# Optimization experiments

Hardware: AMD Instinct MI355X
Metric: run time of the kernel (lower is better)

## Reference

```python
import jax, jax.numpy as jnp
import numpy as np

B, N, D, H = 4, 2048, 768, 12
DH = D // H  # 64


def setup_inputs() -> dict:
    key = jax.random.key(0)
    k1, k2, k3 = jax.random.split(key, 3)
    x = jax.random.normal(k1, (B, N, D), dtype=jnp.float32)
    # causal mask, broadcastable over (b, h): 1 = keep, 0 = masked
    mask = jnp.tril(jnp.ones((N, N), dtype=jnp.int32))[None, None, :, :]
    w_qkv = jax.random.normal(k2, (D, 3 * D), dtype=jnp.float32) * 0.02
    w_out = jax.random.normal(k3, (D, D), dtype=jnp.float32) * 0.02
    return {"x": x, "mask": mask, "w_qkv": w_qkv, "w_out": w_out}


def reference(x, mask, w_qkv, w_out):
    b, n, d = x.shape
    qkv = x @ w_qkv                               # [b, n, 3d]
    q, k, v = jnp.split(qkv, 3, axis=-1)
    def to_heads(t):
        return t.reshape(b, n, H, DH).transpose(0, 2, 1, 3)  # [b, h, n, dh]
    q, k, v = to_heads(q), to_heads(k), to_heads(v)
    attn = jnp.einsum('bhqd,bhkd->bhqk', q, k) / jnp.sqrt(jnp.float32(DH))
    attn = jnp.where(mask == 0, -jnp.inf, attn)
    attn = jax.nn.softmax(attn.astype(jnp.float32), axis=-1).astype(x.dtype)
    out = jnp.einsum('bhqk,bhkd->bhqd', attn, v)  # [b, h, n, dh]
    out = out.transpose(0, 2, 1, 3).reshape(b, n, d)
    return out @ w_out
```

## Files before the change

kernel.cpp:

```cpp
#include <hip/hip_runtime.h>
#include <stdint.h>

#define B_  4
#define N_  2048
#define D_  768
#define H_  12
#define DH_ 64
#define TD  (3*D_)
#define M_  (B_*N_)

typedef __bf16 bf16x8 __attribute__((ext_vector_type(8)));
typedef float  f32x4  __attribute__((ext_vector_type(4)));
typedef unsigned int   u32x4 __attribute__((ext_vector_type(4)));
typedef unsigned short u16x4 __attribute__((ext_vector_type(4)));

__device__ __forceinline__ unsigned short f2bf(float f) {
  union { float f; uint32_t u; } c; c.f = f;
  uint32_t u = c.u;
  uint32_t r = (u + 0x7FFFu + ((u >> 16) & 1u)) >> 16;
  return (unsigned short)r;
}

template <bool A_BF16, bool OUT_BF16>
__global__ __launch_bounds__(256)
void gemm_kernel(const void* __restrict__ Av, const float* __restrict__ Bm,
                 void* __restrict__ Cv, int M, int N, int K,
                 float qscale, int qcols) {
  __shared__ unsigned short As[128 * 32];
  __shared__ unsigned short Bs[128 * 32];
  const int tid  = threadIdx.x;
  const int lane = tid & 63;
  const int wave = tid >> 6;
  const int wr = wave >> 1, wc = wave & 1;
  const int l15 = lane & 15, lh = lane >> 4;
  const int row0 = blockIdx.y * 128;
  const int col0 = blockIdx.x * 128;

  f32x4 acc[4][4] = {};

  for (int k0 = 0; k0 < K; k0 += 32) {
    if constexpr (A_BF16) {
      const unsigned short* A = (const unsigned short*)Av;
      #pragma unroll
      for (int it = 0; it < 2; ++it) {
        int idx = tid + it * 256;
        int r = idx >> 2, c8 = idx & 3;
        u32x4 v = *(const u32x4*)(A + (size_t)(row0 + r) * K + k0 + c8 * 8);
        *(u32x4*)(As + r * 32 + ((c8 * 8) ^ ((r & 6) << 2))) = v;
      }
    } else {
      const float* A = (const float*)Av;
      #pragma unroll
      for (int it = 0; it < 4; ++it) {
        int idx = tid + it * 256;
        int r = idx >> 3, c4 = idx & 7;
        f32x4 v = *(const f32x4*)(A + (size_t)(row0 + r) * K + k0 + c4 * 4);
        u16x4 hx; hx.x = f2bf(v.x); hx.y = f2bf(v.y); hx.z = f2bf(v.z); hx.w = f2bf(v.w);
        *(u16x4*)(As + r * 32 + ((c4 * 4) ^ ((r & 6) << 2))) = hx;
      }
    }
    #pragma unroll
    for (int it = 0; it < 4; ++it) {
      int idx = tid + it * 256;
      int n = idx & 127, kq = idx >> 7;
      float f0 = Bm[(size_t)(k0 + kq * 4 + 0) * N + col0 + n];
      float f1 = Bm[(size_t)(k0 + kq * 4 + 1) * N + col0 + n];
      float f2 = Bm[(size_t)(k0 + kq * 4 + 2) * N + col0 + n];
      float f3 = Bm[(size_t)(k0 + kq * 4 + 3) * N + col0 + n];
      u16x4 hx; hx.x = f2bf(f0); hx.y = f2bf(f1); hx.z = f2bf(f2); hx.w = f2bf(f3);
      *(u16x4*)(Bs + n * 32 + ((kq * 4) ^ ((n & 6) << 2))) = hx;
    }
    __syncthreads();

    bf16x8 af[4], bfv[4];
    #pragma unroll
    for (int mf = 0; mf < 4; ++mf) {
      int rr = wr * 64 + mf * 16 + l15;
      af[mf] = *(const bf16x8*)(As + rr * 32 + ((lh * 8) ^ ((rr & 6) << 2)));
    }
    #pragma unroll
    for (int nf = 0; nf < 4; ++nf) {
      int n = wc * 64 + nf * 16 + l15;
      bfv[nf] = *(const bf16x8*)(Bs + n * 32 + ((lh * 8) ^ ((n & 6) << 2)));
    }
    __builtin_amdgcn_s_setprio(1);
    #pragma unroll
    for (int mf = 0; mf < 4; ++mf)
      #pragma unroll
      for (int nf = 0; nf < 4; ++nf)
        acc[mf][nf] = __builtin_amdgcn_mfma_f32_16x16x32_bf16(af[mf], bfv[nf], acc[mf][nf], 0, 0, 0);
    __builtin_amdgcn_s_setprio(0);
    __syncthreads();
  }

  #pragma unroll
  for (int mf = 0; mf < 4; ++mf) {
    #pragma unroll
    for (int nf = 0; nf < 4; ++nf) {
      #pragma unroll
      for (int rg = 0; rg < 4; ++rg) {
        int rr = row0 + wr * 64 + mf * 16 + lh * 4 + rg;
        int cc = col0 + wc * 64 + nf * 16 + l15;
        float v = acc[mf][nf][rg];
        if (cc < qcols) v *= qscale;
        if constexpr (OUT_BF16) ((unsigned short*)Cv)[(size_t)rr * N + cc] = f2bf(v);
        else                    ((float*)Cv)[(size_t)rr * N + cc] = v;
      }
    }
  }
}

__global__ __launch_bounds__(256)
void attn_kernel(const unsigned short* __restrict__ qkv,
                 float* __restrict__ Oacc, float* __restrict__ Lacc) {
  __shared__ unsigned short Ks[2][64 * 64];
  __shared__ unsigned short Vs[2][64 * 64];
  __shared__ unsigned short Ps[4 * 32 * 64];
  const int tid  = threadIdx.x;
  const int lane = tid & 63, wave = tid >> 6;
  const int l15 = lane & 15, lh = lane >> 4;

  const int g = blockIdx.x;
  const int j = g >> 3;
  const int bh = (j / 40) * 8 + (g & 7);
  const int r = j % 40;
  const int b = bh / H_, h = bh % H_;
  const short cum[17] = {0,1,2,3,4,6,8,10,12,15,18,21,24,28,32,36,40};
  int qb = 15;
  #pragma unroll
  for (int q = 15; q > 0; --q) if (r < cum[q]) qb = q - 1;
  const int chunk = r - cum[qb];
  const int t0 = chunk * 8;
  const int t1 = min(t0 + 8, 2 * (qb + 1));
  const int q0 = qb * 128 + wave * 32;

  bf16x8 qf[2][2];
  #pragma unroll
  for (int mf = 0; mf < 2; ++mf)
    #pragma unroll
    for (int ks = 0; ks < 2; ++ks)
      qf[mf][ks] = *(const bf16x8*)(qkv + (size_t)(b * N_ + q0 + mf * 16 + l15) * TD
                                    + h * DH_ + ks * 32 + lh * 8);

  f32x4 o[2][4] = {};
  float ls[2][4] = {};

  u32x4 kr[2], vr[2];
  const int s_kv = tid >> 3, s_d8 = tid & 7;

  auto ISSUE = [&](int t) {
    #pragma unroll
    for (int it = 0; it < 2; ++it) {
      int kv = s_kv + it * 32;
      size_t base = (size_t)(b * N_ + t * 64 + kv) * TD + h * DH_ + s_d8 * 8;
      kr[it] = *(const u32x4*)(qkv + base + D_);
      vr[it] = *(const u32x4*)(qkv + base + 2 * D_);
    }
  };
  auto WRITE = [&](int buf) {
    #pragma unroll
    for (int it = 0; it < 2; ++it) {
      int kv = s_kv + it * 32;
      *(u32x4*)(&Ks[buf][kv * 64 + ((s_d8 * 8) ^ ((kv & 7) << 3))]) = kr[it];
      const unsigned short* vsp = (const unsigned short*)&vr[it];
      #pragma unroll
      for (int jj = 0; jj < 8; ++jj) {
        int d = s_d8 * 8 + jj;
        int swz = (jj ^ s_d8) & 7;
        Vs[buf][d * 64 + (kv ^ (swz << 3))] = vsp[jj];
      }
    }
  };

  ISSUE(t0); WRITE(0); __syncthreads();

  for (int t = t0; t < t1; ++t) {
    const int cur = (t - t0) & 1;
    const bool more = (t + 1 < t1);
    if (more) ISSUE(t + 1);

    const int kv0 = t * 64;
    if (kv0 <= q0 + 31) {
      f32x4 s[2][4] = {};
      __builtin_amdgcn_s_setprio(1);
      #pragma unroll
      for (int ks = 0; ks < 2; ++ks) {
        bf16x8 kf[4];
        #pragma unroll
        for (int nf = 0; nf < 4; ++nf) {
          int kv = nf * 16 + l15;
          kf[nf] = *(const bf16x8*)(&Ks[cur][kv * 64 + ((ks * 32 + lh * 8) ^ ((kv & 7) << 3))]);
        }
        #pragma unroll
        for (int mf = 0; mf < 2; ++mf)
          #pragma unroll
          for (int nf = 0; nf < 4; ++nf)
            s[mf][nf] = __builtin_amdgcn_mfma_f32_16x16x32_bf16(qf[mf][ks], kf[nf], s[mf][nf], 0, 0, 0);
      }
      __builtin_amdgcn_s_setprio(0);

      const bool need_mask = (kv0 + 63 > q0);
      #pragma unroll
      for (int mf = 0; mf < 2; ++mf) {
        #pragma unroll
        for (int rg = 0; rg < 4; ++rg) {
          const int row = q0 + mf * 16 + lh * 4 + rg;
          const int prow = mf * 16 + lh * 4 + rg;
          float lacc = 0.f;
          #pragma unroll
          for (int nf = 0; nf < 4; ++nf) {
            int col = kv0 + nf * 16 + l15;
            float p = exp2f(s[mf][nf][rg]);
            if (need_mask && col > row) p = 0.f;
            lacc += p;
            Ps[wave * 2048 + prow * 64 + ((nf * 16 + l15) ^ ((prow & 7) << 3))] = f2bf(p);
          }
          ls[mf][rg] += lacc;
        }
      }

      __builtin_amdgcn_s_setprio(1);
      #pragma unroll
      for (int ks = 0; ks < 2; ++ks) {
        bf16x8 pf[2], vf[4];
        #pragma unroll
        for (int mf = 0; mf < 2; ++mf) {
          int pr = mf * 16 + l15;
          pf[mf] = *(const bf16x8*)(&Ps[wave * 2048 + pr * 64 + ((ks * 32 + lh * 8) ^ ((pr & 7) << 3))]);
        }
        #pragma unroll
        for (int nf = 0; nf < 4; ++nf) {
          int d = nf * 16 + l15;
          int swz = ((d & 7) ^ ((d >> 3) & 7)) & 7;
          vf[nf] = *(const bf16x8*)(&Vs[cur][d * 64 + ((ks * 32 + lh * 8) ^ (swz << 3))]);
        }
        #pragma unroll
        for (int mf = 0; mf < 2; ++mf)
          #pragma unroll
          for (int nf = 0; nf < 4; ++nf)
            o[mf][nf] = __builtin_amdgcn_mfma_f32_16x16x32_bf16(pf[mf], vf[nf], o[mf][nf], 0, 0, 0);
      }
      __builtin_amdgcn_s_setprio(0);
    }

    if (more) WRITE(cur ^ 1);
    __syncthreads();
  }

  #pragma unroll
  for (int mf = 0; mf < 2; ++mf)
    #pragma unroll
    for (int rg = 0; rg < 4; ++rg) {
      float v = ls[mf][rg];
      v += __shfl_xor(v, 1); v += __shfl_xor(v, 2);
      v += __shfl_xor(v, 4); v += __shfl_xor(v, 8);
      ls[mf][rg] = v;
    }
  if (l15 == 0) {
    #pragma unroll
    for (int rg = 0; rg < 4; ++rg)
      atomicAdd(&Lacc[(size_t)(b * N_ + q0 + lh * 4 + rg) * H_ + h], ls[0][rg]);
  } else if (l15 == 8) {
    #pragma unroll
    for (int rg = 0; rg < 4; ++rg)
      atomicAdd(&Lacc[(size_t)(b * N_ + q0 + 16 + lh * 4 + rg) * H_ + h], ls[1][rg]);
  }
  #pragma unroll
  for (int mf = 0; mf < 2; ++mf)
    #pragma unroll
    for (int rg = 0; rg < 4; ++rg) {
      int row = q0 + mf * 16 + lh * 4 + rg;
      #pragma unroll
      for (int nf = 0; nf < 4; ++nf)
        atomicAdd(&Oacc[(size_t)(b * N_ + row) * D_ + h * DH_ + nf * 16 + l15], o[mf][nf][rg]);
    }
}

__global__ __launch_bounds__(256)
void norm_kernel(const float* __restrict__ Oacc, const float* __restrict__ Lacc,
                 unsigned short* __restrict__ ctx) {
  int e8 = blockIdx.x * 256 + threadIdx.x;
  int row = e8 / 96, c8 = e8 % 96;
  int h = c8 >> 3;
  float inv = 1.f / Lacc[(size_t)row * H_ + h];
  const float* src = Oacc + (size_t)row * D_ + c8 * 8;
  f32x4 a = *(const f32x4*)(src);
  f32x4 bb = *(const f32x4*)(src + 4);
  u16x4 lo, hi;
  lo.x = f2bf(a.x * inv); lo.y = f2bf(a.y * inv); lo.z = f2bf(a.z * inv); lo.w = f2bf(a.w * inv);
  hi.x = f2bf(bb.x * inv); hi.y = f2bf(bb.y * inv); hi.z = f2bf(bb.z * inv); hi.w = f2bf(bb.w * inv);
  unsigned short* dst = ctx + (size_t)row * D_ + c8 * 8;
  *(u16x4*)(dst) = lo;
  *(u16x4*)(dst + 4) = hi;
}

extern "C" void kernel_launch(void* const* d_in, const int* in_sizes, int n_in,
                              void* d_out, int out_size, void* d_ws, size_t ws_size,
                              hipStream_t stream) {
  const float* x     = (const float*)d_in[0];
  const float* w_qkv = (const float*)d_in[2];
  const float* w_out = (const float*)d_in[3];

  char* ws = (char*)d_ws;
  unsigned short* qkv = (unsigned short*)ws;
  unsigned short* ctx = (unsigned short*)(ws + 37748736);
  float* Lacc         = (float*)(ws + 50331648);
  float* Oacc = (float*)d_out;
  float* out  = (float*)d_out;

  const float SC = 0.18033688011112042f;
  hipMemsetAsync(Oacc, 0, 25165824, stream);
  hipMemsetAsync(Lacc, 0, 393216, stream);

  dim3 blk(256);
  gemm_kernel<false, true><<<dim3(TD / 128, M_ / 128), blk, 0, stream>>>(
      x, w_qkv, qkv, M_, TD, D_, SC, D_);
  attn_kernel<<<dim3(48 * 40), blk, 0, stream>>>(qkv, Oacc, Lacc);
  norm_kernel<<<dim3(M_ * 96 / 256), blk, 0, stream>>>(Oacc, Lacc, ctx);
  gemm_kernel<true, false><<<dim3(D_ / 128, M_ / 128), blk, 0, stream>>>(
      ctx, w_out, out, M_, D_, D_, 1.0f, 0);
}
```

Baseline: 310.8 us.

## Pre-convert inputs to bf16, transpose weights, use direct global-to-LDS GEMM loads

Adds pre-pass kernels that convert x to bf16 and transpose and convert both weight matrices to bf16, folding the Q scale into the transposed QKV weights. The two GEMMs become a single bf16 kernel with both operands K-contiguous, loaded by global_load_lds straight into LDS with a 64-wide K step and an XOR swizzle. This removes the strided fp32 weight gathers and per-element conversions from the GEMM inner loop. It costs three extra launches and more workspace, and it stages x_bf in the output buffer, which is zeroed only after the first GEMM has read it.

```diff
diff --git a/kernel.cpp b/kernel.cpp
--- a/kernel.cpp
+++ b/kernel.cpp
@@ -21,13 +21,55 @@
   return (unsigned short)r;
 }
 
-template <bool A_BF16, bool OUT_BF16>
-__global__ __launch_bounds__(256)
-void gemm_kernel(const void* __restrict__ Av, const float* __restrict__ Bm,
-                 void* __restrict__ Cv, int M, int N, int K,
-                 float qscale, int qcols) {
-  __shared__ unsigned short As[128 * 32];
-  __shared__ unsigned short Bs[128 * 32];
+__device__ __forceinline__ void gload16(const unsigned short* g, unsigned short* l) {
+  __builtin_amdgcn_global_load_lds(
+      (const __attribute__((address_space(1))) void*)g,
+      (__attribute__((address_space(3))) void*)l, 16, 0, 0);
+}
+
+__global__ __launch_bounds__(256)
+void convx_kernel(const float* __restrict__ x, unsigned short* __restrict__ xb) {
+  int i = (blockIdx.x * 256 + threadIdx.x) * 8;
+  f32x4 a = *(const f32x4*)(x + i);
+  f32x4 b = *(const f32x4*)(x + i + 4);
+  u16x4 lo, hi;
+  lo.x = f2bf(a.x); lo.y = f2bf(a.y); lo.z = f2bf(a.z); lo.w = f2bf(a.w);
+  hi.x = f2bf(b.x); hi.y = f2bf(b.y); hi.z = f2bf(b.z); hi.w = f2bf(b.w);
+  *(u16x4*)(xb + i) = lo;
+  *(u16x4*)(xb + i + 4) = hi;
+}
+
+__global__ __launch_bounds__(256)
+void convwT_kernel(const float* __restrict__ W, unsigned short* __restrict__ WT,
+                   int R, int C, float sc, int qcols) {
+  __shared__ float tile[32][33];
+  const int C0 = blockIdx.x * 32, R0 = blockIdx.y * 32;
+  const int t = threadIdx.x;
+  {
+    int r = t >> 3, c4 = (t & 7) * 4;
+    f32x4 v = *(const f32x4*)(W + (size_t)(R0 + r) * C + C0 + c4);
+    tile[r][c4] = v.x; tile[r][c4 + 1] = v.y; tile[r][c4 + 2] = v.z; tile[r][c4 + 3] = v.w;
+  }
+  __syncthreads();
+  {
+    int n = t >> 3, r4 = (t & 7) * 4;
+    float s = (C0 + n) < qcols ? sc : 1.0f;
+    u16x4 o;
+    o.x = f2bf(tile[r4][n] * s);
+    o.y = f2bf(tile[r4 + 1][n] * s);
+    o.z = f2bf(tile[r4 + 2][n] * s);
+    o.w = f2bf(tile[r4 + 3][n] * s);
+    *(u16x4*)(WT + (size_t)(C0 + n) * R + R0 + r4) = o;
+  }
+}
+
+template <bool OUT_BF16>
+__global__ __launch_bounds__(256)
+void gemm_bt_kernel(const unsigned short* __restrict__ A,
+                    const unsigned short* __restrict__ BT,
+                    void* __restrict__ Cv, int M, int N, int K) {
+  __shared__ unsigned short As[128 * 64];
+  __shared__ unsigned short Bs[128 * 64];
   const int tid  = threadIdx.x;
   const int lane = tid & 63;
   const int wave = tid >> 6;
@@ -36,60 +78,52 @@
   const int row0 = blockIdx.y * 128;
   const int col0 = blockIdx.x * 128;
 
+  const unsigned short* ga[4];
+  const unsigned short* gb[4];
+  unsigned short* la = As + wave * 2048;
+  unsigned short* lb = Bs + wave * 2048;
+  #pragma unroll
+  for (int q = 0; q < 4; ++q) {
+    int rl = 32 * wave + 8 * q + (lane >> 3);
+    int kb = (((lane & 7) << 4) ^ ((rl & 7) << 4)) >> 1;
+    ga[q] = A  + (size_t)(row0 + rl) * K + kb;
+    gb[q] = BT + (size_t)(col0 + rl) * K + kb;
+  }
+
   f32x4 acc[4][4] = {};
 
-  for (int k0 = 0; k0 < K; k0 += 32) {
-    if constexpr (A_BF16) {
-      const unsigned short* A = (const unsigned short*)Av;
-      #pragma unroll
-      for (int it = 0; it < 2; ++it) {
-        int idx = tid + it * 256;
-        int r = idx >> 2, c8 = idx & 3;
-        u32x4 v = *(const u32x4*)(A + (size_t)(row0 + r) * K + k0 + c8 * 8);
-        *(u32x4*)(As + r * 32 + ((c8 * 8) ^ ((r & 6) << 2))) = v;
-      }
-    } else {
-      const float* A = (const float*)Av;
-      #pragma unroll
-      for (int it = 0; it < 4; ++it) {
-        int idx = tid + it * 256;
-        int r = idx >> 3, c4 = idx & 7;
-        f32x4 v = *(const f32x4*)(A + (size_t)(row0 + r) * K + k0 + c4 * 4);
-        u16x4 hx; hx.x = f2bf(v.x); hx.y = f2bf(v.y); hx.z = f2bf(v.z); hx.w = f2bf(v.w);
-        *(u16x4*)(As + r * 32 + ((c4 * 4) ^ ((r & 6) << 2))) = hx;
-      }
-    }
-    #pragma unroll
-    for (int it = 0; it < 4; ++it) {
-      int idx = tid + it * 256;
-      int n = idx & 127, kq = idx >> 7;
-      float f0 = Bm[(size_t)(k0 + kq * 4 + 0) * N + col0 + n];
-      float f1 = Bm[(size_t)(k0 + kq * 4 + 1) * N + col0 + n];
-      float f2 = Bm[(size_t)(k0 + kq * 4 + 2) * N + col0 + n];
-      float f3 = Bm[(size_t)(k0 + kq * 4 + 3) * N + col0 + n];
-      u16x4 hx; hx.x = f2bf(f0); hx.y = f2bf(f1); hx.z = f2bf(f2); hx.w = f2bf(f3);
-      *(u16x4*)(Bs + n * 32 + ((kq * 4) ^ ((n & 6) << 2))) = hx;
+  for (int k0 = 0; k0 < K; k0 += 64) {
+    #pragma unroll
+    for (int q = 0; q < 4; ++q) {
+      gload16(ga[q], la + q * 512);
+      gload16(gb[q], lb + q * 512);
+      ga[q] += 64; gb[q] += 64;
     }
     __syncthreads();
 
-    bf16x8 af[4], bfv[4];
-    #pragma unroll
-    for (int mf = 0; mf < 4; ++mf) {
-      int rr = wr * 64 + mf * 16 + l15;
-      af[mf] = *(const bf16x8*)(As + rr * 32 + ((lh * 8) ^ ((rr & 6) << 2)));
-    }
-    #pragma unroll
-    for (int nf = 0; nf < 4; ++nf) {
-      int n = wc * 64 + nf * 16 + l15;
-      bfv[nf] = *(const bf16x8*)(Bs + n * 32 + ((lh * 8) ^ ((n & 6) << 2)));
-    }
-    __builtin_amdgcn_s_setprio(1);
-    #pragma unroll
-    for (int mf = 0; mf < 4; ++mf)
-      #pragma unroll
-      for (int nf = 0; nf < 4; ++nf)
-        acc[mf][nf] = __builtin_amdgcn_mfma_f32_16x16x32_bf16(af[mf], bfv[nf], acc[mf][nf], 0, 0, 0);
-    __builtin_amdgcn_s_setprio(0);
+    #pragma unroll
+    for (int ks = 0; ks < 2; ++ks) {
+      bf16x8 af[4], bfv[4];
+      #pragma unroll
+      for (int mf = 0; mf < 4; ++mf) {
+        int r = wr * 64 + mf * 16 + l15;
+        af[mf] = *(const bf16x8*)((const char*)As +
+                  ((r * 128 + ks * 64 + lh * 16) ^ ((r & 7) << 4)));
+      }
+      #pragma unroll
+      for (int nf = 0; nf < 4; ++nf) {
+        int n = wc * 64 + nf * 16 + l15;
+        bfv[nf] = *(const bf16x8*)((const char*)Bs +
+                  ((n * 128 + ks * 64 + lh * 16) ^ ((n & 7) << 4)));
+      }
+      __builtin_amdgcn_s_setprio(1);
+      #pragma unroll
+      for (int mf = 0; mf < 4; ++mf)
+        #pragma unroll
+        for (int nf = 0; nf < 4; ++nf)
+          acc[mf][nf] = __builtin_amdgcn_mfma_f32_16x16x32_bf16(af[mf], bfv[nf], acc[mf][nf], 0, 0, 0);
+      __builtin_amdgcn_s_setprio(0);
+    }
     __syncthreads();
   }
 
@@ -102,7 +136,6 @@
         int rr = row0 + wr * 64 + mf * 16 + lh * 4 + rg;
         int cc = col0 + wc * 64 + nf * 16 + l15;
         float v = acc[mf][nf][rg];
-        if (cc < qcols) v *= qscale;
         if constexpr (OUT_BF16) ((unsigned short*)Cv)[(size_t)rr * N + cc] = f2bf(v);
         else                    ((float*)Cv)[(size_t)rr * N + cc] = v;
       }
@@ -305,18 +338,22 @@
   unsigned short* qkv = (unsigned short*)ws;
   unsigned short* ctx = (unsigned short*)(ws + 37748736);
   float* Lacc         = (float*)(ws + 50331648);
+  unsigned short* wTq = (unsigned short*)(ws + 50724864);
+  unsigned short* wTo = (unsigned short*)(ws + 54263808);
+  unsigned short* x_bf = (unsigned short*)d_out;
   float* Oacc = (float*)d_out;
   float* out  = (float*)d_out;
 
   const float SC = 0.18033688011112042f;
+  dim3 blk(256);
+
+  convx_kernel<<<dim3(M_ * D_ / 2048), blk, 0, stream>>>(x, x_bf);
+  convwT_kernel<<<dim3(TD / 32, D_ / 32), blk, 0, stream>>>(w_qkv, wTq, D_, TD, SC, D_);
+  convwT_kernel<<<dim3(D_ / 32, D_ / 32), blk, 0, stream>>>(w_out, wTo, D_, D_, 1.0f, 0);
+  hipMemsetAsync(Lacc, 0, 393216, stream);
+  gemm_bt_kernel<true><<<dim3(TD / 128, M_ / 128), blk, 0, stream>>>(x_bf, wTq, qkv, M_, TD, D_);
   hipMemsetAsync(Oacc, 0, 25165824, stream);
-  hipMemsetAsync(Lacc, 0, 393216, stream);
-
-  dim3 blk(256);
-  gemm_kernel<false, true><<<dim3(TD / 128, M_ / 128), blk, 0, stream>>>(
-      x, w_qkv, qkv, M_, TD, D_, SC, D_);
   attn_kernel<<<dim3(48 * 40), blk, 0, stream>>>(qkv, Oacc, Lacc);
   norm_kernel<<<dim3(M_ * 96 / 256), blk, 0, stream>>>(Oacc, Lacc, ctx);
-  gemm_kernel<true, false><<<dim3(D_ / 128, M_ / 128), blk, 0, stream>>>(
-      ctx, w_out, out, M_, D_, D_, 1.0f, 0);
-}
+  gemm_bt_kernel<false><<<dim3(D_ / 128, M_ / 128), blk, 0, stream>>>(ctx, wTo, out, M_, D_, D_);
+}
```

Result: faster. 290.8 us (-6.5%).
